# Optimization experiments

Hardware: AMD Instinct MI355X
Metric: run time of the kernel (lower is better)

The kernel has to match this reference:

```python
import jax, jax.numpy as jnp
import numpy as np

B, T, V, E, H, D = 2048, 50, 65, 100, 20, 5  # batch, block, vocab, n_embd, heads, head_size


def setup_inputs() -> dict:
    key = jax.random.key(0)
    ks = jax.random.split(key, 12)
    idx = jax.random.randint(ks[0], (B, T), 0, V)
    targets = jax.random.randint(ks[1], (B, T), 0, V)
    tok_emb = jax.random.normal(ks[2], (V, E), dtype=jnp.float32) * 0.02
    pos_emb = jax.random.normal(ks[3], (T, E), dtype=jnp.float32) * 0.02
    # per-head Linear(N_EMBD, head_size, bias=False) weights, stacked over heads: [H, D, E]
    Wk = jax.random.normal(ks[4], (H, D, E), dtype=jnp.float32) * 0.1
    Wq = jax.random.normal(ks[5], (H, D, E), dtype=jnp.float32) * 0.1
    Wv = jax.random.normal(ks[6], (H, D, E), dtype=jnp.float32) * 0.1
    W_ff = jax.random.normal(ks[7], (E, E), dtype=jnp.float32) * 0.1
    b_ff = jnp.zeros((E,), dtype=jnp.float32)
    W_lm = jax.random.normal(ks[8], (V, E), dtype=jnp.float32) * 0.1
    b_lm = jnp.zeros((V,), dtype=jnp.float32)
    return {"idx": idx, "targets": targets, "tok_emb": tok_emb, "pos_emb": pos_emb,
            "Wk": Wk, "Wq": Wq, "Wv": Wv, "W_ff": W_ff, "b_ff": b_ff,
            "W_lm": W_lm, "b_lm": b_lm}


def reference(idx, targets, tok_emb, pos_emb, Wk, Wq, Wv, W_ff, b_ff, W_lm, b_lm):
    Bs, Ts = idx.shape
    x = tok_emb[idx] + pos_emb[:Ts]  # [B, T, E]
    # batched over all heads (equivalent to the per-head Python loop + concat)
    k = jnp.einsum('bte,hde->bhtd', x, Wk)
    q = jnp.einsum('bte,hde->bhtd', x, Wq)
    v = jnp.einsum('bte,hde->bhtd', x, Wv)
    # NOTE: faithful to original: k @ q^T, scaled by C**0.5 (multiply, C = N_EMBD)
    scale = jnp.asarray(E, x.dtype) ** 0.5
    w = jnp.einsum('bhtd,bhsd->bhts', k, q) * scale  # [B, H, T, S]
    tril = jnp.tril(jnp.ones((Ts, Ts), dtype=bool))
    w = jnp.where(tril, w, -jnp.inf)
    # original: torch.softmax(weights, dim=1) on [B, T, S] -> axis 't' here (axis=2)
    w = jax.nn.softmax(w, axis=2)
    attn = jnp.einsum('bhts,bhsd->bhtd', w, v)
    attn = attn.transpose(0, 2, 1, 3).reshape(Bs, Ts, H * D)  # concat heads -> [B, T, E]
    h = jax.nn.relu(attn @ W_ff.T + b_ff)  # FeedForward applied AFTER attention
    logits = h @ W_lm.T + b_lm  # [B, T, V]
    logits2d = logits.reshape(Bs * Ts, V)
    tflat = targets.reshape(Bs * Ts)
    logp = jax.nn.log_softmax(logits2d, axis=-1)
    loss = -jnp.take_along_axis(logp, tflat[:, None], axis=-1).mean()
    return (logits2d, loss)
```

## Files before the change

### kernel.cpp

```cpp
#include <hip/hip_runtime.h>
#include <hip/hip_bf16.h>

#define Bb 2048
#define Tt 50
#define Vv 65
#define Ee 100
#define Hh 20
#define Dd 5

typedef __bf16 v8bf __attribute__((ext_vector_type(8)));
typedef short v8s __attribute__((ext_vector_type(8)));
typedef short v4s __attribute__((ext_vector_type(4)));
typedef float f32x4 __attribute__((ext_vector_type(4)));

__device__ __forceinline__ v8bf bzero8() {
    v8s z = {0, 0, 0, 0, 0, 0, 0, 0};
    union { v8s s; v8bf b; } u; u.s = z; return u.b;
}
__device__ __forceinline__ unsigned short bfbits(float f) {
    union { __hip_bfloat16 h; unsigned short s; } c;
    c.h = __float2bfloat16(f);
    return c.s;
}
__device__ __forceinline__ float bf2f(short s) {
    union { unsigned i; float f; } c; c.i = ((unsigned)(unsigned short)s) << 16; return c.f;
}
__device__ __forceinline__ unsigned pack2(float a, float b) {
    return (unsigned)bfbits(a) | ((unsigned)bfbits(b) << 16);
}

__device__ __forceinline__ f32x4 mfma_16x16x16_bf16(v4s a, v4s b, f32x4 c) {
#if __has_builtin(__builtin_amdgcn_mfma_f32_16x16x16bf16_1k)
    return __builtin_amdgcn_mfma_f32_16x16x16bf16_1k(a, b, c, 0, 0, 0);
#else
    f32x4 d;
    asm volatile("v_mfma_f32_16x16x16_bf16 %0, %1, %2, %3\n\ts_nop 7\n\ts_nop 4"
                 : "=v"(d) : "v"(a), "v"(b), "v"(c));
    return d;
#endif
}

#define WS_WKQV 1024
#define WS_WFF  (1024 + 81920)
#define WS_WLM  (1024 + 81920 + 32768)

#define XSTR 136
#define R2 8000
#define R3 16000
#define VSTR 52

__global__ __launch_bounds__(256) void prep_kernel(
    const float* __restrict__ Wk, const float* __restrict__ Wq,
    const float* __restrict__ Wv, const float* __restrict__ Wff,
    const float* __restrict__ Wlm, char* __restrict__ ws,
    float* __restrict__ out)
{
    int g = blockIdx.x * 256 + threadIdx.x;
    if (g == 0) out[Bb * Tt * Vv] = 0.f;
    __hip_bfloat16* wkqv = (__hip_bfloat16*)(ws + WS_WKQV);
    __hip_bfloat16* wff  = (__hip_bfloat16*)(ws + WS_WFF);
    __hip_bfloat16* wlm  = (__hip_bfloat16*)(ws + WS_WLM);
    if (g < 40960) {
        int n = g >> 7, e = g & 127;
        float v = 0.f;
        if (e < Ee) {
            if (n < 100)      v = Wk[n * Ee + e] * 14.4269504089f;
            else if (n < 200) v = Wq[(n - 100) * Ee + e];
            else if (n < 300) v = Wv[(n - 200) * Ee + e];
        }
        wkqv[g] = __float2bfloat16(v);
    } else if (g < 57344) {
        int gg = g - 40960; int n = gg >> 7, e = gg & 127;
        float v = (e < Ee && n < Ee) ? Wff[n * Ee + e] : 0.f;
        wff[gg] = __float2bfloat16(v);
    } else {
        int gg = g - 57344; int n = gg >> 7, e = gg & 127;
        float v = (e < Ee && n < Vv) ? Wlm[n * Ee + e] : 0.f;
        wlm[gg] = __float2bfloat16(v);
    }
}

__global__ __launch_bounds__(256, 3) void gpt_main(
    const int* __restrict__ idx, const int* __restrict__ targets,
    const float* __restrict__ tok_emb, const float* __restrict__ pos_emb,
    const float* __restrict__ b_ff, const float* __restrict__ b_lm,
    const char* __restrict__ ws, float* __restrict__ out)
{
    __shared__ __attribute__((aligned(16))) __hip_bfloat16 sh[21200];
    __shared__ int tok_s[Tt];
    __shared__ float bsum;

    const int b    = blockIdx.x;
    const int tid  = threadIdx.x;
    const int wave = tid >> 6;
    const int ln   = tid & 15;
    const int quad = (tid >> 4) & 3;

    if (tid < Tt) tok_s[tid] = idx[b * Tt + tid];
    if (tid == 0) bsum = 0.f;
    {
        const uint4 z4 = make_uint4(0u, 0u, 0u, 0u);
        for (int i = tid; i < 2650; i += 256) ((uint4*)sh)[i] = z4;
    }
    __syncthreads();
    for (int i = tid; i < Tt * 25; i += 256) {
        int r = i / 25, c4 = (i - r * 25) * 4;
        const float4 te = *(const float4*)&tok_emb[tok_s[r] * Ee + c4];
        const float4 pe = *(const float4*)&pos_emb[r * Ee + c4];
        ushort4 o;
        o.x = bfbits(te.x + pe.x); o.y = bfbits(te.y + pe.y);
        o.z = bfbits(te.z + pe.z); o.w = bfbits(te.w + pe.w);
        *(ushort4*)&sh[r * XSTR + c4] = o;
    }
    __syncthreads();

    {
        const __hip_bfloat16* wkqv = (const __hip_bfloat16*)(ws + WS_WKQV);
        f32x4 acc[5][4];
#pragma unroll
        for (int j = 0; j < 5; ++j)
#pragma unroll
            for (int mt = 0; mt < 4; ++mt) {
                f32x4 z = {0.f, 0.f, 0.f, 0.f};
                acc[j][mt] = z;
            }
#pragma unroll
        for (int kt = 0; kt < 4; ++kt) {
            v8bf a[4];
#pragma unroll
            for (int mt = 0; mt < 4; ++mt)
                a[mt] = (mt < 3 || ln < 2)
                      ? *(const v8bf*)&sh[(mt * 16 + ln) * XSTR + kt * 32 + quad * 8]
                      : bzero8();
#pragma unroll
            for (int j = 0; j < 5; ++j) {
                int nt = wave * 5 + j;
                v8bf bfr = *(const v8bf*)&wkqv[(nt * 16 + ln) * 128 + kt * 32 + quad * 8];
#pragma unroll
                for (int mt = 0; mt < 4; ++mt)
                    acc[j][mt] = __builtin_amdgcn_mfma_f32_16x16x32_bf16(a[mt], bfr, acc[j][mt], 0, 0, 0);
            }
        }
        __syncthreads();
        for (int i = tid; i < 1000; i += 256) {
            *(unsigned short*)&sh[i * 8 + 5] = 0;
            *(unsigned*)&sh[i * 8 + 6] = 0;
        }
#pragma unroll
        for (int j = 0; j < 5; ++j) {
            int n = (wave * 5 + j) * 16 + ln;
            if (n < 300) {
                int mat = n / 100;
                int jj  = n - mat * 100;
                int h   = jj / 5, d = jj - (jj / 5) * 5;
                if (mat == 2) {
                    int base = R3 + (h * 5 + d) * VSTR;
#pragma unroll
                    for (int mt = 0; mt < 4; ++mt) {
                        if (mt < 3 || quad == 0) {
                            float v0 = acc[j][mt][0], v1 = acc[j][mt][1];
                            float v2 = acc[j][mt][2], v3 = acc[j][mt][3];
                            if (mt == 3) { v2 = 0.f; v3 = 0.f; }
                            uint2 pk = make_uint2(pack2(v0, v1), pack2(v2, v3));
                            *(uint2*)&sh[base + mt * 16 + quad * 4] = pk;
                        }
                    }
                } else {
                    int roff = (mat == 0) ? R2 : 0;
                    int rbase = h * 50;
#pragma unroll
                    for (int mt = 0; mt < 4; ++mt)
#pragma unroll
                        for (int r = 0; r < 4; ++r) {
                            int m = mt * 16 + quad * 4 + r;
                            if (m < Tt)
                                sh[roff + (rbase + m) * 8 + d] = __float2bfloat16(acc[j][mt][r]);
                        }
                }
            }
        }
    }
    __syncthreads();

    unsigned attp[5][8];
    {
        const float BIGF = 3.0e38f;
        float dA2[4], dA1[4], d50[4];
#pragma unroll
        for (int r = 0; r < 4; ++r) {
            int qr = quad * 4 + r;
            dA2[r] = (qr >= ln) ? BIGF : 0.f;
            dA1[r] = (ln >= qr) ? BIGF : 0.f;
            d50[r] = (qr < 2)  ? BIGF : 0.f;
        }
        const float tl3 = (ln < 2) ? BIGF : 0.f;

        v4s ones4; ones4[0] = ones4[1] = ones4[2] = ones4[3] = (short)0x3F80;
#pragma unroll
        for (int hj = 0; hj < 5; ++hj) {
            const int h = wave * 5 + hj;
            v8bf qf[4], kf[4];
#pragma unroll
            for (int i = 0; i < 4; ++i) {
                int row = i * 16 + ln;
                qf[i] = (quad == 0) ? *(const v8bf*)&sh[(h * 50 + row) * 8] : bzero8();
                kf[i] = (quad == 0) ? *(const v8bf*)&sh[R2 + (h * 50 + row) * 8] : bzero8();
            }
            float rdv[4][4];
#pragma unroll
            for (int ns = 0; ns < 4; ++ns) {
                float esum[4] = {0.f, 0.f, 0.f, 0.f};
#pragma unroll
                for (int mt = ns; mt < 4; ++mt) {
                    f32x4 z = {0.f, 0.f, 0.f, 0.f};
                    f32x4 t2 = __builtin_amdgcn_mfma_f32_16x16x32_bf16(kf[mt], qf[ns], z, 0, 0, 0);
#pragma unroll
                    for (int r = 0; r < 4; ++r) {
                        float x = __builtin_amdgcn_exp2f(t2[r]);
                        if (mt == ns) x = fminf(x, dA2[r]);
                        if (mt == 3)  x = fminf(x, d50[r]);
                        esum[r] += x;
                    }
                }
                v4s af;
                af[0] = (short)bfbits(esum[0]); af[1] = (short)bfbits(esum[1]);
                af[2] = (short)bfbits(esum[2]); af[3] = (short)bfbits(esum[3]);
                f32x4 z = {0.f, 0.f, 0.f, 0.f};
                f32x4 dres = mfma_16x16x16_bf16(af, ones4, z);
#pragma unroll
                for (int r = 0; r < 4; ++r)
                    rdv[ns][r] = (ns < 3 || (quad * 4 + r) < 2)
                               ? __builtin_amdgcn_rcpf(dres[r]) : 0.f;
            }
            f32x4 pac[4];
#pragma unroll
            for (int mt = 0; mt < 4; ++mt) { f32x4 z = {0.f, 0.f, 0.f, 0.f}; pac[mt] = z; }
#pragma unroll
            for (int ms = 0; ms < 4; ++ms) {
                v4s braw;
                if (ln < Dd && (ms < 3 || quad == 0))
                    braw = *(const v4s*)&sh[R3 + (h * 5 + ln) * VSTR + ms * 16 + quad * 4];
                else { v4s zz = {0, 0, 0, 0}; braw = zz; }
                v4s bvt;
#pragma unroll
                for (int j = 0; j < 4; ++j)
                    bvt[j] = (short)bfbits(bf2f(braw[j]) * rdv[ms][j]);
#pragma unroll
                for (int u = 0; u < 4 - ms; ++u) {
                    f32x4 z = {0.f, 0.f, 0.f, 0.f};
                    f32x4 t1 = __builtin_amdgcn_mfma_f32_16x16x32_bf16(qf[ms], kf[ms + u], z, 0, 0, 0);
                    v4s af;
#pragma unroll
                    for (int r = 0; r < 4; ++r) {
                        float x = __builtin_amdgcn_exp2f(t1[r]);
                        if (u == 0)      x = fminf(x, dA1[r]);
                        if (ms + u == 3) x = fminf(x, tl3);
                        if (ms == 3)     x = fminf(x, d50[r]);
                        af[r] = (short)bfbits(x);
                    }
                    pac[ms + u] = mfma_16x16x16_bf16(af, bvt, pac[ms + u]);
                }
            }
#pragma unroll
            for (int mt = 0; mt < 4; ++mt) {
                attp[hj][mt * 2]     = pack2(pac[mt][0], pac[mt][1]);
                attp[hj][mt * 2 + 1] = pack2(pac[mt][2], pac[mt][3]);
            }
        }
    }
    __syncthreads();

#pragma unroll
    for (int hj = 0; hj < 5; ++hj) {
        int col = (wave * 5 + hj) * 5 + ln;
#pragma unroll
        for (int mt = 0; mt < 4; ++mt)
#pragma unroll
            for (int r = 0; r < 4; ++r) {
                int t = mt * 16 + quad * 4 + r;
                if (ln < Dd && t < Tt) {
                    unsigned w = attp[hj][mt * 2 + (r >> 1)];
                    unsigned short v = (unsigned short)((r & 1) ? (w >> 16) : (w & 0xffff));
                    *(unsigned short*)&sh[t * XSTR + col] = v;
                }
            }
    }
    __syncthreads();

    {
        const __hip_bfloat16* wff = (const __hip_bfloat16*)(ws + WS_WFF);
        f32x4 fac[2][4];
#pragma unroll
        for (int u = 0; u < 2; ++u)
#pragma unroll
            for (int mt = 0; mt < 4; ++mt) {
                f32x4 z = {0.f, 0.f, 0.f, 0.f};
                fac[u][mt] = z;
            }
        const int nn = (wave < 3) ? 2 : 1;
#pragma unroll
        for (int kt = 0; kt < 4; ++kt) {
            v8bf a[4];
#pragma unroll
            for (int mt = 0; mt < 4; ++mt)
                a[mt] = (mt < 3 || ln < 2)
                      ? *(const v8bf*)&sh[(mt * 16 + ln) * XSTR + kt * 32 + quad * 8]
                      : bzero8();
#pragma unroll
            for (int u = 0; u < 2; ++u) {
                if (u < nn) {
                    int nt = wave + u * 4;
                    v8bf bfr = *(const v8bf*)&wff[(nt * 16 + ln) * 128 + kt * 32 + quad * 8];
#pragma unroll
                    for (int mt = 0; mt < 4; ++mt)
                        fac[u][mt] = __builtin_amdgcn_mfma_f32_16x16x32_bf16(a[mt], bfr, fac[u][mt], 0, 0, 0);
                }
            }
        }
#pragma unroll
        for (int u = 0; u < 2; ++u) {
            if (u < nn) {
                int n = (wave + u * 4) * 16 + ln;
                if (n < Ee) {
                    float bias = b_ff[n];
#pragma unroll
                    for (int mt = 0; mt < 4; ++mt)
#pragma unroll
                        for (int r = 0; r < 4; ++r) {
                            int m = mt * 16 + quad * 4 + r;
                            if (m < Tt) {
                                float v = fac[u][mt][r] + bias;
                                sh[R2 + m * XSTR + n] = __float2bfloat16(v > 0.f ? v : 0.f);
                            }
                        }
                }
            }
        }
    }
    __syncthreads();

    {
        const __hip_bfloat16* wlm = (const __hip_bfloat16*)(ws + WS_WLM);
        float* lgl = (float*)sh;
#pragma unroll
        for (int i = 0; i < 5; ++i) {
            int job = wave + i * 4;
            int mt = job / 5, nt = job - (job / 5) * 5;
            f32x4 acc = {0.f, 0.f, 0.f, 0.f};
#pragma unroll
            for (int kt = 0; kt < 4; ++kt) {
                v8bf a = (mt < 3 || ln < 2)
                       ? *(const v8bf*)&sh[R2 + (mt * 16 + ln) * XSTR + kt * 32 + quad * 8]
                       : bzero8();
                v8bf bf = *(const v8bf*)&wlm[(nt * 16 + ln) * 128 + kt * 32 + quad * 8];
                acc = __builtin_amdgcn_mfma_f32_16x16x32_bf16(a, bf, acc, 0, 0, 0);
            }
            int n = nt * 16 + ln;
            if (n < Vv) {
                float bias = b_lm[n];
#pragma unroll
                for (int r = 0; r < 4; ++r) {
                    int m = mt * 16 + quad * 4 + r;
                    if (m < Tt) {
                        float v = acc[r] + bias;
                        out[(b * Tt + m) * Vv + n] = v;
                        lgl[m * 68 + n] = v;
                    }
                }
            }
        }
    }
    __syncthreads();

    if (tid < 200) {
        int r = tid >> 2, lv = tid & 3;
        const float* row = (const float*)sh + r * 68;
        float mx = -3.0e38f;
        for (int v = lv; v < Vv; v += 4) mx = fmaxf(mx, row[v]);
        mx = fmaxf(mx, __shfl_xor(mx, 1));
        mx = fmaxf(mx, __shfl_xor(mx, 2));
        float sum = 0.f;
        for (int v = lv; v < Vv; v += 4)
            sum += __builtin_amdgcn_exp2f((row[v] - mx) * 1.4426950408889634f);
        sum += __shfl_xor(sum, 1);
        sum += __shfl_xor(sum, 2);
        if (lv == 0) {
            float lse = mx + 0.69314718055994531f * log2f(sum);
            int tgt = targets[b * Tt + r];
            atomicAdd(&bsum, lse - row[tgt]);
        }
    }
    __syncthreads();
    if (tid == 0)
        atomicAdd(&out[Bb * Tt * Vv], bsum * (1.0f / (float)(Bb * Tt)));
}

extern "C" void kernel_launch(void* const* d_in, const int* in_sizes, int n_in,
                              void* d_out, int out_size, void* d_ws, size_t ws_size,
                              hipStream_t stream)
{
    const int* idx     = (const int*)d_in[0];
    const int* targets = (const int*)d_in[1];
    const float* tok_emb = (const float*)d_in[2];
    const float* pos_emb = (const float*)d_in[3];
    const float* Wk  = (const float*)d_in[4];
    const float* Wq  = (const float*)d_in[5];
    const float* Wv  = (const float*)d_in[6];
    const float* Wff = (const float*)d_in[7];
    const float* bff = (const float*)d_in[8];
    const float* Wlm = (const float*)d_in[9];
    const float* blm = (const float*)d_in[10];
    float* out = (float*)d_out;
    char* ws = (char*)d_ws;

    hipLaunchKernelGGL(prep_kernel, dim3(264), dim3(256), 0, stream, Wk, Wq, Wv, Wff, Wlm, ws, out);
    hipLaunchKernelGGL(gpt_main, dim3(Bb), dim3(256), 0, stream,
                       idx, targets, tok_emb, pos_emb, bff, blm, (const char*)ws, out);
}
```

Baseline: 177.4 us.

## Reuse exponentiated scores for softmax denominators and drop full shared-memory zeroing

The attention loop no longer runs a separate pass of transposed score MFMAs plus exps to build column sums. It computes the score tile once, keeps the exponentiated bf16 fragments for the PV MFMA, and reduces the denominators with cross-lane shuffles. This halves the score MFMA and exp2 work per head, at the cost of more live registers and shuffle traffic. The up-front zeroing of the whole shared buffer is removed; instead the embedding loop writes zero padding columns, and the pad lanes of both the Q and K regions are cleared explicitly.

```diff
diff --git a/kernel.cpp b/kernel.cpp
--- a/kernel.cpp
+++ b/kernel.cpp
@@ -98,18 +98,18 @@
 
     if (tid < Tt) tok_s[tid] = idx[b * Tt + tid];
     if (tid == 0) bsum = 0.f;
-    {
-        const uint4 z4 = make_uint4(0u, 0u, 0u, 0u);
-        for (int i = tid; i < 2650; i += 256) ((uint4*)sh)[i] = z4;
-    }
-    __syncthreads();
-    for (int i = tid; i < Tt * 25; i += 256) {
-        int r = i / 25, c4 = (i - r * 25) * 4;
-        const float4 te = *(const float4*)&tok_emb[tok_s[r] * Ee + c4];
-        const float4 pe = *(const float4*)&pos_emb[r * Ee + c4];
+    __syncthreads();
+    for (int i = tid; i < Tt * 32; i += 256) {
+        int r = i >> 5, c4 = (i & 31) * 4;
         ushort4 o;
-        o.x = bfbits(te.x + pe.x); o.y = bfbits(te.y + pe.y);
-        o.z = bfbits(te.z + pe.z); o.w = bfbits(te.w + pe.w);
+        if (c4 < Ee) {
+            const float4 te = *(const float4*)&tok_emb[tok_s[r] * Ee + c4];
+            const float4 pe = *(const float4*)&pos_emb[r * Ee + c4];
+            o.x = bfbits(te.x + pe.x); o.y = bfbits(te.y + pe.y);
+            o.z = bfbits(te.z + pe.z); o.w = bfbits(te.w + pe.w);
+        } else {
+            o.x = 0; o.y = 0; o.z = 0; o.w = 0;
+        }
         *(ushort4*)&sh[r * XSTR + c4] = o;
     }
     __syncthreads();
@@ -142,9 +142,10 @@
             }
         }
         __syncthreads();
-        for (int i = tid; i < 1000; i += 256) {
-            *(unsigned short*)&sh[i * 8 + 5] = 0;
-            *(unsigned*)&sh[i * 8 + 6] = 0;
+        for (int i = tid; i < 2000; i += 256) {
+            int off = (i < 1000) ? i * 8 : R2 + (i - 1000) * 8;
+            *(unsigned short*)&sh[off + 5] = 0;
+            *(unsigned*)&sh[off + 6] = 0;
         }
 #pragma unroll
         for (int j = 0; j < 5; ++j) {
@@ -185,17 +186,15 @@
     unsigned attp[5][8];
     {
         const float BIGF = 3.0e38f;
-        float dA2[4], dA1[4], d50[4];
+        float dA1[4], d50[4];
 #pragma unroll
         for (int r = 0; r < 4; ++r) {
             int qr = quad * 4 + r;
-            dA2[r] = (qr >= ln) ? BIGF : 0.f;
             dA1[r] = (ln >= qr) ? BIGF : 0.f;
             d50[r] = (qr < 2)  ? BIGF : 0.f;
         }
         const float tl3 = (ln < 2) ? BIGF : 0.f;
 
-        v4s ones4; ones4[0] = ones4[1] = ones4[2] = ones4[3] = (short)0x3F80;
 #pragma unroll
         for (int hj = 0; hj < 5; ++hj) {
             const int h = wave * 5 + hj;
@@ -206,37 +205,43 @@
                 qf[i] = (quad == 0) ? *(const v8bf*)&sh[(h * 50 + row) * 8] : bzero8();
                 kf[i] = (quad == 0) ? *(const v8bf*)&sh[R2 + (h * 50 + row) * 8] : bzero8();
             }
-            float rdv[4][4];
-#pragma unroll
-            for (int ns = 0; ns < 4; ++ns) {
+            f32x4 pac[4];
+#pragma unroll
+            for (int mt = 0; mt < 4; ++mt) { f32x4 z = {0.f, 0.f, 0.f, 0.f}; pac[mt] = z; }
+#pragma unroll
+            for (int ms = 0; ms < 4; ++ms) {
                 float esum[4] = {0.f, 0.f, 0.f, 0.f};
-#pragma unroll
-                for (int mt = ns; mt < 4; ++mt) {
+                v4s afs[4];
+#pragma unroll
+                for (int u = 0; u < 4 - ms; ++u) {
                     f32x4 z = {0.f, 0.f, 0.f, 0.f};
-                    f32x4 t2 = __builtin_amdgcn_mfma_f32_16x16x32_bf16(kf[mt], qf[ns], z, 0, 0, 0);
+                    f32x4 t1 = __builtin_amdgcn_mfma_f32_16x16x32_bf16(qf[ms], kf[ms + u], z, 0, 0, 0);
+                    v4s af;
 #pragma unroll
                     for (int r = 0; r < 4; ++r) {
-                        float x = __builtin_amdgcn_exp2f(t2[r]);
-                        if (mt == ns) x = fminf(x, dA2[r]);
-                        if (mt == 3)  x = fminf(x, d50[r]);
+                        float x = __builtin_amdgcn_exp2f(t1[r]);
+                        if (u == 0)      x = fminf(x, dA1[r]);
+                        if (ms + u == 3) x = fminf(x, tl3);
+                        if (ms == 3)     x = fminf(x, d50[r]);
                         esum[r] += x;
+                        af[r] = (short)bfbits(x);
                     }
-                }
-                v4s af;
-                af[0] = (short)bfbits(esum[0]); af[1] = (short)bfbits(esum[1]);
-                af[2] = (short)bfbits(esum[2]); af[3] = (short)bfbits(esum[3]);
-                f32x4 z = {0.f, 0.f, 0.f, 0.f};
-                f32x4 dres = mfma_16x16x16_bf16(af, ones4, z);
+                    afs[u] = af;
+                }
+#pragma unroll
+                for (int r = 0; r < 4; ++r) {
+                    float e = esum[r];
+                    e += __shfl_xor(e, 1);
+                    e += __shfl_xor(e, 2);
+                    e += __shfl_xor(e, 4);
+                    e += __shfl_xor(e, 8);
+                    esum[r] = e;
+                }
+                float rdv[4];
 #pragma unroll
                 for (int r = 0; r < 4; ++r)
-                    rdv[ns][r] = (ns < 3 || (quad * 4 + r) < 2)
-                               ? __builtin_amdgcn_rcpf(dres[r]) : 0.f;
-            }
-            f32x4 pac[4];
-#pragma unroll
-            for (int mt = 0; mt < 4; ++mt) { f32x4 z = {0.f, 0.f, 0.f, 0.f}; pac[mt] = z; }
-#pragma unroll
-            for (int ms = 0; ms < 4; ++ms) {
+                    rdv[r] = (ms < 3 || (quad * 4 + r) < 2)
+                           ? __builtin_amdgcn_rcpf(esum[r]) : 0.f;
                 v4s braw;
                 if (ln < Dd && (ms < 3 || quad == 0))
                     braw = *(const v4s*)&sh[R3 + (h * 5 + ln) * VSTR + ms * 16 + quad * 4];
@@ -244,22 +249,10 @@
                 v4s bvt;
 #pragma unroll
                 for (int j = 0; j < 4; ++j)
-                    bvt[j] = (short)bfbits(bf2f(braw[j]) * rdv[ms][j]);
-#pragma unroll
-                for (int u = 0; u < 4 - ms; ++u) {
-                    f32x4 z = {0.f, 0.f, 0.f, 0.f};
-                    f32x4 t1 = __builtin_amdgcn_mfma_f32_16x16x32_bf16(qf[ms], kf[ms + u], z, 0, 0, 0);
-                    v4s af;
-#pragma unroll
-                    for (int r = 0; r < 4; ++r) {
-                        float x = __builtin_amdgcn_exp2f(t1[r]);
-                        if (u == 0)      x = fminf(x, dA1[r]);
-                        if (ms + u == 3) x = fminf(x, tl3);
-                        if (ms == 3)     x = fminf(x, d50[r]);
-                        af[r] = (short)bfbits(x);
-                    }
-                    pac[ms + u] = mfma_16x16x16_bf16(af, bvt, pac[ms + u]);
-                }
+                    bvt[j] = (short)bfbits(bf2f(braw[j]) * rdv[j]);
+#pragma unroll
+                for (int u = 0; u < 4 - ms; ++u)
+                    pac[ms + u] = mfma_16x16x16_bf16(afs[u], bvt, pac[ms + u]);
             }
 #pragma unroll
             for (int mt = 0; mt < 4; ++mt) {
```

Result: slower. 181.5 us (+2.3%).
